# Performance work log

Hardware: AMD Instinct MI355X
Metric: run time of the kernel (lower is better)

The kernel has to match this reference:

```python
import jax, jax.numpy as jnp
import numpy as np

B, C, H, W, HEADS = 8, 256, 64, 64, 4
EPS = 1e-5  # torch InstanceNorm2d default eps


def conv1x1(x, w):
    # w: [out_c, in_c]; x: [b, in_c, h, w]
    return jnp.einsum('oc,bchw->bohw', w, x)


def maxpool2(x):
    b, c, h, w = x.shape
    return x.reshape(b, c, h // 2, 2, w // 2, 2).max(axis=(3, 5))


def inorm_affine(x, g, b):
    # InstanceNorm2d(affine=True): normalize per (batch, channel) over H,W
    m = jnp.mean(x, axis=(2, 3), keepdims=True)
    v = jnp.mean((x - m) ** 2, axis=(2, 3), keepdims=True)
    return (x - m) * jax.lax.rsqrt(v + EPS) * g[None, :, None, None] + b[None, :, None, None]


def setup_inputs() -> dict:
    key = jax.random.key(0)
    ks = jax.random.split(key, 12)
    s = 1.0 / np.sqrt(C)  # fan-in style scaling for 1x1 conv weights
    return {
        'x': jax.random.normal(ks[0], (B, C, H, W), jnp.float32),
        'theta_w': jax.random.normal(ks[1], (C, C), jnp.float32) * s,
        'phi_w': jax.random.normal(ks[2], (C, C), jnp.float32) * s,
        'g_w': jax.random.normal(ks[3], (C // 2, C), jnp.float32) * s,
        'o_w': jax.random.normal(ks[4], (C, C // 2), jnp.float32) * np.sqrt(2.0 / C),
        'nt_w': 1.0 + 0.1 * jax.random.normal(ks[5], (C,), jnp.float32),
        'nt_b': 0.1 * jax.random.normal(ks[6], (C,), jnp.float32),
        'np_w': 1.0 + 0.1 * jax.random.normal(ks[7], (C,), jnp.float32),
        'np_b': 0.1 * jax.random.normal(ks[8], (C,), jnp.float32),
        'ng_w': 1.0 + 0.1 * jax.random.normal(ks[9], (C // 2,), jnp.float32),
        'ng_b': 0.1 * jax.random.normal(ks[10], (C // 2,), jnp.float32),
        'gamma': jnp.float32(0.5),
    }


def reference(x, theta_w, phi_w, g_w, o_w, nt_w, nt_b, np_w, np_b, ng_w, ng_b, gamma):
    b, c, h, w = x.shape
    n = h * w            # query length
    m = n // 4           # key/value length after 2x2 maxpool
    theta = inorm_affine(conv1x1(x, theta_w), nt_w, nt_b)
    phi = inorm_affine(maxpool2(conv1x1(x, phi_w)), np_w, np_b)
    g = inorm_affine(maxpool2(conv1x1(x, g_w)), ng_w, ng_b)
    # custom head layout: channel dim split as (C//heads, heads), head dim INNER
    theta_ = theta.reshape(b, c // HEADS, HEADS, n)
    phi_ = phi.reshape(b, c // HEADS, HEADS, m)
    g_ = g.reshape(b, (c // 2) // HEADS, HEADS, m)
    beta = jax.nn.softmax(jnp.einsum('bchi,bchj->bhij', theta_, phi_), axis=-1)
    o = jnp.einsum('bchj,bhij->bchi', g_, beta).reshape(b, c // 2, h, w)
    o = conv1x1(o, o_w)
    return gamma * o + x
```

## Files before the change

### kernel.cpp

```cpp
#include <hip/hip_runtime.h>
#include <hip/hip_bf16.h>
#include <math.h>

typedef float f32x4 __attribute__((ext_vector_type(4)));
typedef float f32x16 __attribute__((ext_vector_type(16)));
typedef __bf16 b16x8 __attribute__((ext_vector_type(8)));
typedef __bf16 b16x4 __attribute__((ext_vector_type(4)));
typedef unsigned int u32x2 __attribute__((ext_vector_type(2)));
typedef unsigned int u32x4 __attribute__((ext_vector_type(4)));

#define L2E 1.44269504088896340736f

__global__ void prep_weights(const float* tw, const float* pw, const float* gw,
                             const float* ow, __bf16* Wp, __bf16* OWp) {
    int idx = blockIdx.x * 256 + threadIdx.x;
    if (idx < 640 * 256) {
        int m = idx >> 8, k = idx & 255;
        float v;
        if (m < 256)      { int o = ((m & 63) << 2) + (m >> 6);            v = tw[o * 256 + k]; }
        else if (m < 512) { int mm = m - 256; int o = ((mm & 63) << 2) + (mm >> 6); v = pw[o * 256 + k]; }
        else              { int mm = m - 512; int o = ((mm & 31) << 2) + (mm >> 5); v = gw[o * 256 + k]; }
        Wp[idx] = (__bf16)v;
    } else {
        int j = idx - 640 * 256;
        if (j < 256 * 128) {
            int m = j >> 7, c = j & 127;
            int o = ((c & 31) << 2) + (c >> 5);
            OWp[j] = (__bf16)ow[m * 128 + o];
        }
    }
}

__global__ void transpose_x(const float* x, __bf16* xt) {
    __shared__ float tile[32][33];
    int b = blockIdx.z, c0 = blockIdx.y * 32, p0 = blockIdx.x * 32;
    int tx = threadIdx.x & 31, ty = threadIdx.x >> 5;
#pragma unroll
    for (int i = 0; i < 4; i++) {
        int cy = ty + i * 8;
        tile[cy][tx] = x[((size_t)(b * 256 + c0 + cy)) * 4096 + p0 + tx];
    }
    __syncthreads();
#pragma unroll
    for (int i = 0; i < 4; i++) {
        int py = ty + i * 8;
        xt[((size_t)b * 4096 + p0 + py) * 256 + c0 + tx] = (__bf16)tile[tx][py];
    }
}

__global__ __launch_bounds__(256) void conv_gemm(const __bf16* __restrict__ Wp,
                                                 const __bf16* __restrict__ xt,
                                                 __bf16* theta_t, __bf16* phi_t, __bf16* g_t) {
    int b = blockIdx.z, mt = blockIdx.y, nt = blockIdx.x;
    __shared__ __bf16 Al[128 * 40];
    __shared__ __bf16 Bl[128 * 40];
    int tid = threadIdx.x, l = tid & 63, w = tid >> 6;
    int wm = w >> 1, wn = w & 1, lr = l & 15, lg = l >> 4;
    f32x4 acc[4][4];
#pragma unroll
    for (int i = 0; i < 4; i++)
#pragma unroll
        for (int j = 0; j < 4; j++)
#pragma unroll
            for (int r = 0; r < 4; r++) acc[i][j][r] = 0.f;
    const __bf16* Ag = Wp + (size_t)mt * 128 * 256;
    const __bf16* Bg = xt + ((size_t)b * 4096 + nt * 128) * 256;
    int srow = tid >> 2, scol = (tid & 3) * 8;
    b16x8 aR[2], bR[2];
#pragma unroll
    for (int hh = 0; hh < 2; hh++) {
        int r = srow + hh * 64;
        aR[hh] = *(const b16x8*)&Ag[(size_t)r * 256 + scol];
        bR[hh] = *(const b16x8*)&Bg[(size_t)r * 256 + scol];
    }
    for (int k0 = 0; k0 < 256; k0 += 32) {
        if (k0) __syncthreads();
#pragma unroll
        for (int hh = 0; hh < 2; hh++) {
            int r = srow + hh * 64;
            *(b16x8*)&Al[r * 40 + scol] = aR[hh];
            *(b16x8*)&Bl[r * 40 + scol] = bR[hh];
        }
        __syncthreads();
        if (k0 < 224) {
#pragma unroll
            for (int hh = 0; hh < 2; hh++) {
                int r = srow + hh * 64;
                aR[hh] = *(const b16x8*)&Ag[(size_t)r * 256 + k0 + 32 + scol];
                bR[hh] = *(const b16x8*)&Bg[(size_t)r * 256 + k0 + 32 + scol];
            }
        }
        int ko = lg * 8;
        b16x8 af[4], bfr[4];
#pragma unroll
        for (int i = 0; i < 4; i++) af[i]  = *(b16x8*)&Al[(wm * 64 + i * 16 + lr) * 40 + ko];
#pragma unroll
        for (int i = 0; i < 4; i++) bfr[i] = *(b16x8*)&Bl[(wn * 64 + i * 16 + lr) * 40 + ko];
#pragma unroll
        for (int i = 0; i < 4; i++)
#pragma unroll
            for (int j = 0; j < 4; j++)
                acc[i][j] = __builtin_amdgcn_mfma_f32_16x16x32_bf16(af[i], bfr[j], acc[i][j], 0, 0, 0);
    }
    int rbase = lg * 4;
#pragma unroll
    for (int i = 0; i < 4; i++) {
        int m = mt * 128 + wm * 64 + i * 16 + rbase;
#pragma unroll
        for (int j = 0; j < 4; j++) {
            int p = nt * 128 + wn * 64 + j * 16 + lr;
            b16x4 v;
#pragma unroll
            for (int r = 0; r < 4; r++) v[r] = (__bf16)acc[i][j][r];
            if (m < 256)      *(b16x4*)&theta_t[((size_t)b * 4096 + p) * 256 + m] = v;
            else if (m < 512) *(b16x4*)&phi_t[((size_t)b * 4096 + p) * 256 + (m - 256)] = v;
            else              *(b16x4*)&g_t[((size_t)b * 4096 + p) * 128 + (m - 512)] = v;
        }
    }
}

__global__ __launch_bounds__(256) void theta_stats(const __bf16* __restrict__ src,
                                                   float* p1, float* p2) {
    __shared__ float S1[8][256], S2[8][256];
    int b = blockIdx.y, blk = blockIdx.x;
    int tid = threadIdx.x, cg = tid & 31, rg = tid >> 5;
    float a1[8], a2[8];
#pragma unroll
    for (int e = 0; e < 8; e++) { a1[e] = 0.f; a2[e] = 0.f; }
    const __bf16* base = src + ((size_t)b * 4096 + blk * 64 + rg * 8) * 256 + cg * 8;
#pragma unroll
    for (int r = 0; r < 8; r++) {
        b16x8 v = *(const b16x8*)&base[(size_t)r * 256];
#pragma unroll
        for (int e = 0; e < 8; e++) { float f = (float)v[e]; a1[e] += f; a2[e] += f * f; }
    }
#pragma unroll
    for (int e = 0; e < 8; e++) { S1[rg][cg * 8 + e] = a1[e]; S2[rg][cg * 8 + e] = a2[e]; }
    __syncthreads();
    float s1 = 0.f, s2 = 0.f;
#pragma unroll
    for (int i = 0; i < 8; i++) { s1 += S1[i][tid]; s2 += S2[i][tid]; }
    p1[(b * 64 + blk) * 256 + tid] = s1;
    p2[(b * 64 + blk) * 256 + tid] = s2;
}

__global__ __launch_bounds__(256) void pool_phi(const __bf16* __restrict__ src, __bf16* dst,
                                                float* p1, float* p2) {
    __shared__ float S1[8][256], S2[8][256];
    int b = blockIdx.y, qc = blockIdx.x;
    int tid = threadIdx.x, cg = tid & 31, qg = tid >> 5;
    float a1[8], a2[8];
#pragma unroll
    for (int e = 0; e < 8; e++) { a1[e] = 0.f; a2[e] = 0.f; }
#pragma unroll
    for (int qq = 0; qq < 4; qq++) {
        int q = qc * 32 + qg * 4 + qq, qy = q >> 5, qx = q & 31;
        size_t base = ((size_t)(b * 4096) + qy * 128 + qx * 2) * 256 + cg * 8;
        b16x8 v0 = *(const b16x8*)&src[base];
        b16x8 v1 = *(const b16x8*)&src[base + 256];
        b16x8 v2 = *(const b16x8*)&src[base + 16384];
        b16x8 v3 = *(const b16x8*)&src[base + 16640];
        b16x8 mv;
#pragma unroll
        for (int e = 0; e < 8; e++) {
            float m = fmaxf(fmaxf((float)v0[e], (float)v1[e]), fmaxf((float)v2[e], (float)v3[e]));
            mv[e] = (__bf16)m; a1[e] += m; a2[e] += m * m;
        }
        *(b16x8*)&dst[((size_t)b * 1024 + q) * 256 + cg * 8] = mv;
    }
#pragma unroll
    for (int e = 0; e < 8; e++) { S1[qg][cg * 8 + e] = a1[e]; S2[qg][cg * 8 + e] = a2[e]; }
    __syncthreads();
    float s1 = 0.f, s2 = 0.f;
#pragma unroll
    for (int i = 0; i < 8; i++) { s1 += S1[i][tid]; s2 += S2[i][tid]; }
    p1[(b * 32 + qc) * 256 + tid] = s1;
    p2[(b * 32 + qc) * 256 + tid] = s2;
}

__global__ __launch_bounds__(256) void pool_gT(const __bf16* __restrict__ src, __bf16* gT,
                                               float* p1, float* p2) {
    __shared__ __bf16 Pt[64][136];
    __shared__ float S1[16][128], S2[16][128];
    int b = blockIdx.y, qc = blockIdx.x;
    int tid = threadIdx.x, cg = tid & 15, qg = tid >> 4;
    float a1[8], a2[8];
#pragma unroll
    for (int e = 0; e < 8; e++) { a1[e] = 0.f; a2[e] = 0.f; }
#pragma unroll
    for (int qq = 0; qq < 4; qq++) {
        int ql = qg * 4 + qq, q = qc * 64 + ql;
        int qy = q >> 5, qx = q & 31;
        size_t base = ((size_t)(b * 4096) + qy * 128 + qx * 2) * 128 + cg * 8;
        b16x8 v0 = *(const b16x8*)&src[base];
        b16x8 v1 = *(const b16x8*)&src[base + 128];
        b16x8 v2 = *(const b16x8*)&src[base + 8192];
        b16x8 v3 = *(const b16x8*)&src[base + 8320];
        b16x8 mv;
#pragma unroll
        for (int e = 0; e < 8; e++) {
            float m = fmaxf(fmaxf((float)v0[e], (float)v1[e]), fmaxf((float)v2[e], (float)v3[e]));
            mv[e] = (__bf16)m; a1[e] += m; a2[e] += m * m;
        }
        *(b16x8*)&Pt[ql][cg * 8] = mv;
    }
#pragma unroll
    for (int e = 0; e < 8; e++) { S1[qg][cg * 8 + e] = a1[e]; S2[qg][cg * 8 + e] = a2[e]; }
    __syncthreads();
    if (tid < 128) {
        float s1 = 0.f, s2 = 0.f;
#pragma unroll
        for (int i = 0; i < 16; i++) { s1 += S1[i][tid]; s2 += S2[i][tid]; }
        p1[(b * 16 + qc) * 128 + tid] = s1;
        p2[(b * 16 + qc) * 128 + tid] = s2;
    }
    int c = tid & 127, qh = tid >> 7;
    int hh = c >> 5, ch = c & 31;
#pragma unroll
    for (int sg = 0; sg < 4; sg++) {
        int seg = qh * 4 + sg;
        b16x8 v;
#pragma unroll
        for (int e = 0; e < 8; e++) v[e] = Pt[seg * 8 + e][c];
        *(b16x8*)&gT[((((size_t)(b * 4 + hh) * 16 + qc) * 8 + seg) * 32 + ch) * 8] = v;
    }
}

__global__ void finalize_stats(const float* tp1, const float* tp2, const float* pp1,
                               const float* pp2, const float* gp1, const float* gp2,
                               const float* ntw, const float* ntb, const float* npw,
                               const float* npb, const float* ngw, const float* ngb,
                               float* sct, float* bit, float* scp, float* bip,
                               float* scg, float* big) {
    int idx = blockIdx.x * 256 + threadIdx.x;
    if (idx >= 8 * 640) return;
    int b = idx / 640, c = idx % 640;
    if (c < 256) {
        float s1 = 0.f, s2 = 0.f;
        for (int i = 0; i < 64; i++) { s1 += tp1[(b * 64 + i) * 256 + c]; s2 += tp2[(b * 64 + i) * 256 + c]; }
        float n = 4096.f;
        float m = s1 / n, v = s2 / n - m * m;
        float r = rsqrtf(v + 1e-5f);
        int o = ((c & 63) << 2) + (c >> 6);
        float wv = ntw[o], bv = ntb[o];
        sct[b * 256 + c] = r * wv * L2E;
        bit[b * 256 + c] = (bv - m * r * wv) * L2E;
    } else if (c < 512) {
        int cc = c - 256;
        float s1 = 0.f, s2 = 0.f;
        for (int i = 0; i < 32; i++) { s1 += pp1[(b * 32 + i) * 256 + cc]; s2 += pp2[(b * 32 + i) * 256 + cc]; }
        float n = 1024.f;
        float m = s1 / n, v = s2 / n - m * m;
        float r = rsqrtf(v + 1e-5f);
        int o = ((cc & 63) << 2) + (cc >> 6);
        float wv = npw[o], bv = npb[o];
        scp[b * 256 + cc] = r * wv; bip[b * 256 + cc] = bv - m * r * wv;
    } else {
        int cc = c - 512;
        float s1 = 0.f, s2 = 0.f;
        for (int i = 0; i < 16; i++) { s1 += gp1[(b * 16 + i) * 128 + cc]; s2 += gp2[(b * 16 + i) * 128 + cc]; }
        float n = 1024.f;
        float m = s1 / n, v = s2 / n - m * m;
        float r = rsqrtf(v + 1e-5f);
        int o = ((cc & 31) << 2) + (cc >> 5);
        float wv = ngw[o], bv = ngb[o];
        scg[b * 128 + cc] = r * wv; big[b * 128 + cc] = bv - m * r * wv;
    }
}

__global__ void normalize_phi(const __bf16* __restrict__ php, __bf16* __restrict__ phk,
                              const float* __restrict__ scp, const float* __restrict__ bip) {
    int blk = blockIdx.x, t = threadIdx.x;
    int b = blk >> 6, h = (blk >> 4) & 3, cc = blk & 15;
#pragma unroll
    for (int uu = 0; uu < 2; uu++) {
        int u = uu * 256 + t;
        int slot = u >> 6, key = u & 63;
        int q = cc * 64 + key;
        int cfull = h * 64 + (slot >> 1) * 16 + (slot & 1) * 8;
        b16x8 v = *(const b16x8*)&php[((size_t)b * 1024 + q) * 256 + cfull];
        b16x8 nv;
#pragma unroll
        for (int e = 0; e < 8; e++)
            nv[e] = (__bf16)((float)v[e] * scp[b * 256 + cfull + e] + bip[b * 256 + cfull + e]);
        *(b16x8*)&phk[((((size_t)(b * 4 + h) * 16 + cc) * 8 + slot) * 64 + key) * 8] = nv;
    }
}

__global__ __launch_bounds__(256, 2) void attn(const __bf16* __restrict__ theta_t,
                                               const __bf16* __restrict__ phk,
                                               const __bf16* __restrict__ gTz,
                                               const float* __restrict__ sct,
                                               const float* __restrict__ bit,
                                               const float* __restrict__ scg,
                                               const float* __restrict__ big,
                                               __bf16* __restrict__ o_mid) {
    __shared__ __bf16 Kb[2][4096];
    __shared__ __bf16 Vb[2][2048];
    int bid = blockIdx.x;
    int idx = bid >> 3;
    int bh = (bid & 7) * 4 + (idx >> 4), qt = idx & 15;
    int b = bh >> 2, h = bh & 3;
    int tid = threadIdx.x, w = tid >> 6, lane = tid & 63;
    int l31 = lane & 31, hi = lane >> 5;
    int qb = qt * 256 + w * 64;

    b16x8 qf[2][4];
#pragma unroll
    for (int m = 0; m < 2; m++) {
        int q = qb + m * 32 + l31;
        const __bf16* qp = theta_t + ((size_t)b * 4096 + q) * 256 + h * 64;
#pragma unroll
        for (int st = 0; st < 4; st++) {
            int cb = st * 16 + hi * 8;
            b16x8 raw = *(const b16x8*)&qp[cb];
            b16x8 nv;
#pragma unroll
            for (int e = 0; e < 8; e++) {
                int cix = b * 256 + h * 64 + cb + e;
                nv[e] = (__bf16)((float)raw[e] * sct[cix] + bit[cix]);
            }
            qf[m][st] = nv;
        }
    }

    const __bf16* Kg = phk + (size_t)bh * 65536;
    const __bf16* Vg = gTz + (size_t)bh * 32768;

    f32x16 oacc[2];
    float l_run[2] = {0.f, 0.f};
#pragma unroll
    for (int m = 0; m < 2; m++)
#pragma unroll
        for (int r = 0; r < 16; r++) oacc[m][r] = 0.f;
    f32x16 zc;
#pragma unroll
    for (int r = 0; r < 16; r++) zc[r] = 0.f;

#define ISSUE(buf, cc) { \
    __builtin_amdgcn_global_load_lds( \
        (const __attribute__((address_space(1))) void*)(Kg + (size_t)(cc) * 4096 + (w * 2) * 512 + lane * 8), \
        (__attribute__((address_space(3))) void*)(&Kb[buf][(w * 2) * 512]), 16, 0, 0); \
    __builtin_amdgcn_global_load_lds( \
        (const __attribute__((address_space(1))) void*)(Kg + (size_t)(cc) * 4096 + (w * 2 + 1) * 512 + lane * 8), \
        (__attribute__((address_space(3))) void*)(&Kb[buf][(w * 2 + 1) * 512]), 16, 0, 0); \
    __builtin_amdgcn_global_load_lds( \
        (const __attribute__((address_space(1))) void*)(Vg + (size_t)(cc) * 2048 + w * 512 + lane * 8), \
        (__attribute__((address_space(3))) void*)(&Vb[buf][w * 512]), 16, 0, 0); }

#define COMPUTE(cur) { \
    b16x8 ak[2][4], av[4]; \
    _Pragma("unroll") for (int kf = 0; kf < 2; kf++) \
    _Pragma("unroll") for (int st = 0; st < 4; st++) \
        ak[kf][st] = *(b16x8*)&Kb[cur][(st * 2 + hi) * 512 + (kf * 32 + l31) * 8]; \
    _Pragma("unroll") for (int js = 0; js < 4; js++) \
        av[js] = *(b16x8*)&Vb[cur][((js * 2 + hi) * 32 + l31) * 8]; \
    _Pragma("unroll") for (int m = 0; m < 2; m++) { \
        _Pragma("unroll") for (int kf = 0; kf < 2; kf++) { \
            f32x16 s = __builtin_amdgcn_mfma_f32_32x32x16_bf16(ak[kf][0], qf[m][0], zc, 0, 0, 0); \
            _Pragma("unroll") for (int st = 1; st < 4; st++) \
                s = __builtin_amdgcn_mfma_f32_32x32x16_bf16(ak[kf][st], qf[m][st], s, 0, 0, 0); \
            float s0 = 0.f, s1 = 0.f, s2p = 0.f, s3 = 0.f; \
            _Pragma("unroll") for (int r = 0; r < 16; r += 4) { \
                float p0 = __builtin_amdgcn_exp2f(s[r]); \
                float p1 = __builtin_amdgcn_exp2f(s[r + 1]); \
                float p2 = __builtin_amdgcn_exp2f(s[r + 2]); \
                float p3 = __builtin_amdgcn_exp2f(s[r + 3]); \
                s[r] = p0; s[r + 1] = p1; s[r + 2] = p2; s[r + 3] = p3; \
                s0 += p0; s1 += p1; s2p += p2; s3 += p3; \
            } \
            l_run[m] += (s0 + s1) + (s2p + s3); \
            _Pragma("unroll") for (int hh2 = 0; hh2 < 2; hh2++) { \
                b16x4 A4, B4; \
                _Pragma("unroll") for (int e = 0; e < 4; e++) { \
                    A4[e] = (__bf16)s[hh2 * 8 + e]; B4[e] = (__bf16)s[hh2 * 8 + 4 + e]; } \
                u32x2 a2 = __builtin_bit_cast(u32x2, A4); \
                u32x2 b2 = __builtin_bit_cast(u32x2, B4); \
                u32x2 q0 = __builtin_amdgcn_permlane32_swap(a2[0], b2[0], false, false); \
                u32x2 q1 = __builtin_amdgcn_permlane32_swap(a2[1], b2[1], false, false); \
                u32x4 pd = {q0[0], q1[0], q0[1], q1[1]}; \
                b16x8 pf = __builtin_bit_cast(b16x8, pd); \
                oacc[m] = __builtin_amdgcn_mfma_f32_32x32x16_bf16(av[kf * 2 + hh2], pf, oacc[m], 0, 0, 0); \
            } \
        } \
    } }

    ISSUE(0, 0)
    __syncthreads();
#pragma unroll 1
    for (int c = 0; c < 16; c++) {
        if (c < 15) ISSUE((c + 1) & 1, c + 1)
        COMPUTE(c & 1)
        __syncthreads();
    }
#undef ISSUE
#undef COMPUTE

#pragma unroll
    for (int m = 0; m < 2; m++) {
        float lr = l_run[m] + __shfl_xor(l_run[m], 32, 64);
        float rl = 1.0f / lr;
        int q = qb + m * 32 + l31;
#pragma unroll
        for (int rr = 0; rr < 4; rr++) {
            b16x4 v;
#pragma unroll
            for (int e = 0; e < 4; e++) {
                int ci = b * 128 + h * 32 + rr * 8 + hi * 4 + e;
                v[e] = (__bf16)(oacc[m][rr * 4 + e] * rl * scg[ci] + big[ci]);
            }
            *(b16x4*)&o_mid[((size_t)b * 4096 + q) * 128 + h * 32 + rr * 8 + hi * 4] = v;
        }
    }
}

__global__ __launch_bounds__(256) void out_gemm(const __bf16* __restrict__ OWp,
                                                const __bf16* __restrict__ o_mid,
                                                const float* __restrict__ x,
                                                const float* gamma, float* out) {
    int b = blockIdx.z, mt = blockIdx.y, nt = blockIdx.x;
    __shared__ __bf16 Al[128 * 40];
    __shared__ __bf16 Bl[128 * 40];
    int tid = threadIdx.x, l = tid & 63, w = tid >> 6;
    int wm = w >> 1, wn = w & 1, lr = l & 15, lg = l >> 4;
    f32x4 acc[4][4];
#pragma unroll
    for (int i = 0; i < 4; i++)
#pragma unroll
        for (int j = 0; j < 4; j++)
#pragma unroll
            for (int r = 0; r < 4; r++) acc[i][j][r] = 0.f;
    const __bf16* Ag = OWp + (size_t)mt * 128 * 128;
    const __bf16* Bg = o_mid + ((size_t)b * 4096 + nt * 128) * 128;
    int srow = tid >> 2, scol = (tid & 3) * 8;
    b16x8 aR[2], bR[2];
#pragma unroll
    for (int hh = 0; hh < 2; hh++) {
        int r = srow + hh * 64;
        aR[hh] = *(const b16x8*)&Ag[(size_t)r * 128 + scol];
        bR[hh] = *(const b16x8*)&Bg[(size_t)r * 128 + scol];
    }
    for (int k0 = 0; k0 < 128; k0 += 32) {
        if (k0) __syncthreads();
#pragma unroll
        for (int hh = 0; hh < 2; hh++) {
            int r = srow + hh * 64;
            *(b16x8*)&Al[r * 40 + scol] = aR[hh];
            *(b16x8*)&Bl[r * 40 + scol] = bR[hh];
        }
        __syncthreads();
        if (k0 < 96) {
#pragma unroll
            for (int hh = 0; hh < 2; hh++) {
                int r = srow + hh * 64;
                aR[hh] = *(const b16x8*)&Ag[(size_t)r * 128 + k0 + 32 + scol];
                bR[hh] = *(const b16x8*)&Bg[(size_t)r * 128 + k0 + 32 + scol];
            }
        }
        int ko = lg * 8;
        b16x8 af[4], bfr[4];
#pragma unroll
        for (int i = 0; i < 4; i++) af[i]  = *(b16x8*)&Al[(wm * 64 + i * 16 + lr) * 40 + ko];
#pragma unroll
        for (int i = 0; i < 4; i++) bfr[i] = *(b16x8*)&Bl[(wn * 64 + i * 16 + lr) * 40 + ko];
#pragma unroll
        for (int i = 0; i < 4; i++)
#pragma unroll
            for (int j = 0; j < 4; j++)
                acc[i][j] = __builtin_amdgcn_mfma_f32_16x16x32_bf16(af[i], bfr[j], acc[i][j], 0, 0, 0);
    }
    float gm = gamma[0];
    int rbase = lg * 4;
#pragma unroll
    for (int i = 0; i < 4; i++) {
        int m = mt * 128 + wm * 64 + i * 16 + rbase;
#pragma unroll
        for (int j = 0; j < 4; j++) {
            int p = nt * 128 + wn * 64 + j * 16 + lr;
#pragma unroll
            for (int r = 0; r < 4; r++) {
                size_t o = ((size_t)b * 256 + m + r) * 4096 + p;
                out[o] = gm * acc[i][j][r] + x[o];
            }
        }
    }
}

extern "C" void kernel_launch(void* const* d_in, const int* in_sizes, int n_in,
                              void* d_out, int out_size, void* d_ws, size_t ws_size,
                              hipStream_t stream) {
    const float* x   = (const float*)d_in[0];
    const float* tw  = (const float*)d_in[1];
    const float* pw  = (const float*)d_in[2];
    const float* gw  = (const float*)d_in[3];
    const float* ow  = (const float*)d_in[4];
    const float* ntw = (const float*)d_in[5];
    const float* ntb = (const float*)d_in[6];
    const float* npw = (const float*)d_in[7];
    const float* npb = (const float*)d_in[8];
    const float* ngw = (const float*)d_in[9];
    const float* ngb = (const float*)d_in[10];
    const float* gamma = (const float*)d_in[11];
    float* out = (float*)d_out;
    char* ws = (char*)d_ws;

    __bf16* Wp  = (__bf16*)(ws + 0);
    __bf16* OWp = (__bf16*)(ws + 327680);
    __bf16* xt  = (__bf16*)(ws + 393216);
    __bf16* th  = (__bf16*)(ws + 17170432);
    __bf16* phr = (__bf16*)(ws + 33947648);
    __bf16* ghr = (__bf16*)(ws + 50724864);
    __bf16* php = (__bf16*)(ws + 59113472);
    __bf16* gT  = (__bf16*)(ws + 63307776);
    float* sb   = (float*)(ws + 65445888);

    float* tp1 = (float*)(ws + 393216);
    float* tp2 = (float*)(ws + 917504);
    float* pp1 = (float*)(ws + 1441792);
    float* pp2 = (float*)(ws + 1703936);
    float* gp1 = (float*)(ws + 1966080);
    float* gp2 = (float*)(ws + 2031616);
    __bf16* phk = phr;
    __bf16* om  = xt;

    float *sct = sb, *bit = sb + 2048, *scp = sb + 4096, *bip = sb + 6144,
          *scg = sb + 8192, *big = sb + 9216;

    prep_weights<<<768, 256, 0, stream>>>(tw, pw, gw, ow, Wp, OWp);
    transpose_x<<<dim3(128, 8, 8), 256, 0, stream>>>(x, xt);
    conv_gemm<<<dim3(32, 5, 8), 256, 0, stream>>>(Wp, xt, th, phr, ghr);
    theta_stats<<<dim3(64, 8), 256, 0, stream>>>(th, tp1, tp2);
    pool_phi<<<dim3(32, 8), 256, 0, stream>>>(phr, php, pp1, pp2);
    pool_gT<<<dim3(16, 8), 256, 0, stream>>>(ghr, gT, gp1, gp2);
    finalize_stats<<<20, 256, 0, stream>>>(tp1, tp2, pp1, pp2, gp1, gp2,
                                           ntw, ntb, npw, npb, ngw, ngb,
                                           sct, bit, scp, bip, scg, big);
    normalize_phi<<<512, 256, 0, stream>>>(php, phk, scp, bip);
    attn<<<512, 256, 0, stream>>>(th, phk, gT, sct, bit, scg, big, om);
    out_gemm<<<dim3(32, 2, 8), 256, 0, stream>>>(OWp, om, x, gamma, out);
}
```

Measured before the change: 124.5 us.

## Fuse x transpose into conv GEMM and triple-buffer attention with smaller query tiles

Removes the separate transpose_x kernel: conv_gemm now reads fp32 x directly in channel-major order, converts it to bf16 and writes the transposed tile into LDS. The attention kernel halves the query tile per wave (one 32-row fragment instead of two), doubling the grid to 1024 blocks. It also switches K/V staging to a three-buffer ring with explicit vmcnt waits and a single barrier per step. This cuts a full-tensor round trip and aims to improve latency hiding and occupancy. The cost is more K/V reloads per query and less reuse of each loaded tile.

After: 120.2 us. 1.04x faster.

```diff
diff --git a/kernel.cpp b/kernel.cpp
--- a/kernel.cpp
+++ b/kernel.cpp
@@ -31,25 +31,8 @@
     }
 }
 
-__global__ void transpose_x(const float* x, __bf16* xt) {
-    __shared__ float tile[32][33];
-    int b = blockIdx.z, c0 = blockIdx.y * 32, p0 = blockIdx.x * 32;
-    int tx = threadIdx.x & 31, ty = threadIdx.x >> 5;
-#pragma unroll
-    for (int i = 0; i < 4; i++) {
-        int cy = ty + i * 8;
-        tile[cy][tx] = x[((size_t)(b * 256 + c0 + cy)) * 4096 + p0 + tx];
-    }
-    __syncthreads();
-#pragma unroll
-    for (int i = 0; i < 4; i++) {
-        int py = ty + i * 8;
-        xt[((size_t)b * 4096 + p0 + py) * 256 + c0 + tx] = (__bf16)tile[tx][py];
-    }
-}
-
 __global__ __launch_bounds__(256) void conv_gemm(const __bf16* __restrict__ Wp,
-                                                 const __bf16* __restrict__ xt,
+                                                 const float* __restrict__ x,
                                                  __bf16* theta_t, __bf16* phi_t, __bf16* g_t) {
     int b = blockIdx.z, mt = blockIdx.y, nt = blockIdx.x;
     __shared__ __bf16 Al[128 * 40];
@@ -64,31 +47,41 @@
 #pragma unroll
             for (int r = 0; r < 4; r++) acc[i][j][r] = 0.f;
     const __bf16* Ag = Wp + (size_t)mt * 128 * 256;
-    const __bf16* Bg = xt + ((size_t)b * 4096 + nt * 128) * 256;
+    const float* Bx = x + (size_t)b * 1048576 + nt * 128;
     int srow = tid >> 2, scol = (tid & 3) * 8;
-    b16x8 aR[2], bR[2];
-#pragma unroll
-    for (int hh = 0; hh < 2; hh++) {
-        int r = srow + hh * 64;
-        aR[hh] = *(const b16x8*)&Ag[(size_t)r * 256 + scol];
-        bR[hh] = *(const b16x8*)&Bg[(size_t)r * 256 + scol];
-    }
+    int bn = tid & 127, bk0 = (tid >> 7) * 8;
+    b16x8 aR[2];
+    float xr[2][8];
+#pragma unroll
+    for (int hh = 0; hh < 2; hh++)
+        aR[hh] = *(const b16x8*)&Ag[(size_t)(srow + hh * 64) * 256 + scol];
+#pragma unroll
+    for (int u = 0; u < 2; u++)
+#pragma unroll
+        for (int e = 0; e < 8; e++)
+            xr[u][e] = Bx[(size_t)(bk0 + u * 16 + e) * 4096 + bn];
     for (int k0 = 0; k0 < 256; k0 += 32) {
         if (k0) __syncthreads();
 #pragma unroll
-        for (int hh = 0; hh < 2; hh++) {
-            int r = srow + hh * 64;
-            *(b16x8*)&Al[r * 40 + scol] = aR[hh];
-            *(b16x8*)&Bl[r * 40 + scol] = bR[hh];
+        for (int hh = 0; hh < 2; hh++)
+            *(b16x8*)&Al[(srow + hh * 64) * 40 + scol] = aR[hh];
+#pragma unroll
+        for (int u = 0; u < 2; u++) {
+            b16x8 v;
+#pragma unroll
+            for (int e = 0; e < 8; e++) v[e] = (__bf16)xr[u][e];
+            *(b16x8*)&Bl[bn * 40 + bk0 + u * 16] = v;
         }
         __syncthreads();
         if (k0 < 224) {
 #pragma unroll
-            for (int hh = 0; hh < 2; hh++) {
-                int r = srow + hh * 64;
-                aR[hh] = *(const b16x8*)&Ag[(size_t)r * 256 + k0 + 32 + scol];
-                bR[hh] = *(const b16x8*)&Bg[(size_t)r * 256 + k0 + 32 + scol];
-            }
+            for (int hh = 0; hh < 2; hh++)
+                aR[hh] = *(const b16x8*)&Ag[(size_t)(srow + hh * 64) * 256 + k0 + 32 + scol];
+#pragma unroll
+            for (int u = 0; u < 2; u++)
+#pragma unroll
+                for (int e = 0; e < 8; e++)
+                    xr[u][e] = Bx[(size_t)(k0 + 32 + bk0 + u * 16 + e) * 4096 + bn];
         }
         int ko = lg * 8;
         b16x8 af[4], bfr[4];
@@ -295,20 +288,18 @@
                                                const float* __restrict__ scg,
                                                const float* __restrict__ big,
                                                __bf16* __restrict__ o_mid) {
-    __shared__ __bf16 Kb[2][4096];
-    __shared__ __bf16 Vb[2][2048];
+    __shared__ __bf16 Kb[3][4096];
+    __shared__ __bf16 Vb[3][2048];
     int bid = blockIdx.x;
     int idx = bid >> 3;
-    int bh = (bid & 7) * 4 + (idx >> 4), qt = idx & 15;
+    int bh = (bid & 7) * 4 + (idx >> 5), qt = idx & 31;
     int b = bh >> 2, h = bh & 3;
     int tid = threadIdx.x, w = tid >> 6, lane = tid & 63;
     int l31 = lane & 31, hi = lane >> 5;
-    int qb = qt * 256 + w * 64;
-
-    b16x8 qf[2][4];
-#pragma unroll
-    for (int m = 0; m < 2; m++) {
-        int q = qb + m * 32 + l31;
+    int q = qt * 128 + w * 32 + l31;
+
+    b16x8 qf[4];
+    {
         const __bf16* qp = theta_t + ((size_t)b * 4096 + q) * 256 + h * 64;
 #pragma unroll
         for (int st = 0; st < 4; st++) {
@@ -320,19 +311,17 @@
                 int cix = b * 256 + h * 64 + cb + e;
                 nv[e] = (__bf16)((float)raw[e] * sct[cix] + bit[cix]);
             }
-            qf[m][st] = nv;
+            qf[st] = nv;
         }
     }
 
     const __bf16* Kg = phk + (size_t)bh * 65536;
     const __bf16* Vg = gTz + (size_t)bh * 32768;
 
-    f32x16 oacc[2];
-    float l_run[2] = {0.f, 0.f};
-#pragma unroll
-    for (int m = 0; m < 2; m++)
-#pragma unroll
-        for (int r = 0; r < 16; r++) oacc[m][r] = 0.f;
+    f32x16 oacc;
+    float l_run = 0.f;
+#pragma unroll
+    for (int r = 0; r < 16; r++) oacc[r] = 0.f;
     f32x16 zc;
 #pragma unroll
     for (int r = 0; r < 16; r++) zc[r] = 0.f;
@@ -355,59 +344,58 @@
         ak[kf][st] = *(b16x8*)&Kb[cur][(st * 2 + hi) * 512 + (kf * 32 + l31) * 8]; \
     _Pragma("unroll") for (int js = 0; js < 4; js++) \
         av[js] = *(b16x8*)&Vb[cur][((js * 2 + hi) * 32 + l31) * 8]; \
-    _Pragma("unroll") for (int m = 0; m < 2; m++) { \
-        _Pragma("unroll") for (int kf = 0; kf < 2; kf++) { \
-            f32x16 s = __builtin_amdgcn_mfma_f32_32x32x16_bf16(ak[kf][0], qf[m][0], zc, 0, 0, 0); \
-            _Pragma("unroll") for (int st = 1; st < 4; st++) \
-                s = __builtin_amdgcn_mfma_f32_32x32x16_bf16(ak[kf][st], qf[m][st], s, 0, 0, 0); \
-            float s0 = 0.f, s1 = 0.f, s2p = 0.f, s3 = 0.f; \
-            _Pragma("unroll") for (int r = 0; r < 16; r += 4) { \
-                float p0 = __builtin_amdgcn_exp2f(s[r]); \
-                float p1 = __builtin_amdgcn_exp2f(s[r + 1]); \
-                float p2 = __builtin_amdgcn_exp2f(s[r + 2]); \
-                float p3 = __builtin_amdgcn_exp2f(s[r + 3]); \
-                s[r] = p0; s[r + 1] = p1; s[r + 2] = p2; s[r + 3] = p3; \
-                s0 += p0; s1 += p1; s2p += p2; s3 += p3; \
-            } \
-            l_run[m] += (s0 + s1) + (s2p + s3); \
-            _Pragma("unroll") for (int hh2 = 0; hh2 < 2; hh2++) { \
-                b16x4 A4, B4; \
-                _Pragma("unroll") for (int e = 0; e < 4; e++) { \
-                    A4[e] = (__bf16)s[hh2 * 8 + e]; B4[e] = (__bf16)s[hh2 * 8 + 4 + e]; } \
-                u32x2 a2 = __builtin_bit_cast(u32x2, A4); \
-                u32x2 b2 = __builtin_bit_cast(u32x2, B4); \
-                u32x2 q0 = __builtin_amdgcn_permlane32_swap(a2[0], b2[0], false, false); \
-                u32x2 q1 = __builtin_amdgcn_permlane32_swap(a2[1], b2[1], false, false); \
-                u32x4 pd = {q0[0], q1[0], q0[1], q1[1]}; \
-                b16x8 pf = __builtin_bit_cast(b16x8, pd); \
-                oacc[m] = __builtin_amdgcn_mfma_f32_32x32x16_bf16(av[kf * 2 + hh2], pf, oacc[m], 0, 0, 0); \
-            } \
+    _Pragma("unroll") for (int kf = 0; kf < 2; kf++) { \
+        f32x16 s = __builtin_amdgcn_mfma_f32_32x32x16_bf16(ak[kf][0], qf[0], zc, 0, 0, 0); \
+        _Pragma("unroll") for (int st = 1; st < 4; st++) \
+            s = __builtin_amdgcn_mfma_f32_32x32x16_bf16(ak[kf][st], qf[st], s, 0, 0, 0); \
+        float s0 = 0.f, s1 = 0.f, s2p = 0.f, s3 = 0.f; \
+        _Pragma("unroll") for (int r = 0; r < 16; r += 4) { \
+            float p0 = __builtin_amdgcn_exp2f(s[r]); \
+            float p1 = __builtin_amdgcn_exp2f(s[r + 1]); \
+            float p2 = __builtin_amdgcn_exp2f(s[r + 2]); \
+            float p3 = __builtin_amdgcn_exp2f(s[r + 3]); \
+            s[r] = p0; s[r + 1] = p1; s[r + 2] = p2; s[r + 3] = p3; \
+            s0 += p0; s1 += p1; s2p += p2; s3 += p3; \
+        } \
+        l_run += (s0 + s1) + (s2p + s3); \
+        _Pragma("unroll") for (int hh2 = 0; hh2 < 2; hh2++) { \
+            b16x4 A4, B4; \
+            _Pragma("unroll") for (int e = 0; e < 4; e++) { \
+                A4[e] = (__bf16)s[hh2 * 8 + e]; B4[e] = (__bf16)s[hh2 * 8 + 4 + e]; } \
+            u32x2 a2 = __builtin_bit_cast(u32x2, A4); \
+            u32x2 b2 = __builtin_bit_cast(u32x2, B4); \
+            u32x2 q0 = __builtin_amdgcn_permlane32_swap(a2[0], b2[0], false, false); \
+            u32x2 q1 = __builtin_amdgcn_permlane32_swap(a2[1], b2[1], false, false); \
+            u32x4 pd = {q0[0], q1[0], q0[1], q1[1]}; \
+            b16x8 pf = __builtin_bit_cast(b16x8, pd); \
+            oacc = __builtin_amdgcn_mfma_f32_32x32x16_bf16(av[kf * 2 + hh2], pf, oacc, 0, 0, 0); \
         } \
     } }
 
     ISSUE(0, 0)
-    __syncthreads();
+    ISSUE(1, 1)
 #pragma unroll 1
     for (int c = 0; c < 16; c++) {
-        if (c < 15) ISSUE((c + 1) & 1, c + 1)
-        COMPUTE(c & 1)
-        __syncthreads();
+        if (c < 15) { asm volatile("s_waitcnt vmcnt(3)" ::: "memory"); }
+        else        { asm volatile("s_waitcnt vmcnt(0)" ::: "memory"); }
+        __builtin_amdgcn_s_barrier();
+        __builtin_amdgcn_sched_barrier(0);
+        if (c + 2 < 16) { int ib = (c + 2) % 3; ISSUE(ib, c + 2) }
+        COMPUTE(c % 3)
     }
 #undef ISSUE
 #undef COMPUTE
 
-#pragma unroll
-    for (int m = 0; m < 2; m++) {
-        float lr = l_run[m] + __shfl_xor(l_run[m], 32, 64);
+    {
+        float lr = l_run + __shfl_xor(l_run, 32, 64);
         float rl = 1.0f / lr;
-        int q = qb + m * 32 + l31;
 #pragma unroll
         for (int rr = 0; rr < 4; rr++) {
             b16x4 v;
 #pragma unroll
             for (int e = 0; e < 4; e++) {
                 int ci = b * 128 + h * 32 + rr * 8 + hi * 4 + e;
-                v[e] = (__bf16)(oacc[m][rr * 4 + e] * rl * scg[ci] + big[ci]);
+                v[e] = (__bf16)(oacc[rr * 4 + e] * rl * scg[ci] + big[ci]);
             }
             *(b16x4*)&o_mid[((size_t)b * 4096 + q) * 128 + h * 32 + rr * 8 + hi * 4] = v;
         }
@@ -506,7 +494,6 @@
 
     __bf16* Wp  = (__bf16*)(ws + 0);
     __bf16* OWp = (__bf16*)(ws + 327680);
-    __bf16* xt  = (__bf16*)(ws + 393216);
     __bf16* th  = (__bf16*)(ws + 17170432);
     __bf16* phr = (__bf16*)(ws + 33947648);
     __bf16* ghr = (__bf16*)(ws + 50724864);
@@ -521,14 +508,13 @@
     float* gp1 = (float*)(ws + 1966080);
     float* gp2 = (float*)(ws + 2031616);
     __bf16* phk = phr;
-    __bf16* om  = xt;
+    __bf16* om  = (__bf16*)(ws + 2097152);
 
     float *sct = sb, *bit = sb + 2048, *scp = sb + 4096, *bip = sb + 6144,
           *scg = sb + 8192, *big = sb + 9216;
 
     prep_weights<<<768, 256, 0, stream>>>(tw, pw, gw, ow, Wp, OWp);
-    transpose_x<<<dim3(128, 8, 8), 256, 0, stream>>>(x, xt);
-    conv_gemm<<<dim3(32, 5, 8), 256, 0, stream>>>(Wp, xt, th, phr, ghr);
+    conv_gemm<<<dim3(32, 5, 8), 256, 0, stream>>>(Wp, x, th, phr, ghr);
     theta_stats<<<dim3(64, 8), 256, 0, stream>>>(th, tp1, tp2);
     pool_phi<<<dim3(32, 8), 256, 0, stream>>>(phr, php, pp1, pp2);
     pool_gT<<<dim3(16, 8), 256, 0, stream>>>(ghr, gT, gp1, gp2);
@@ -536,6 +522,6 @@
                                            ntw, ntb, npw, npb, ngw, ngb,
                                            sct, bit, scp, bip, scg, big);
     normalize_phi<<<512, 256, 0, stream>>>(php, phk, scp, bip);
-    attn<<<512, 256, 0, stream>>>(th, phk, gT, sct, bit, scg, big, om);
+    attn<<<1024, 256, 0, stream>>>(th, phk, gT, sct, bit, scg, big, om);
     out_gemm<<<dim3(32, 2, 8), 256, 0, stream>>>(OWp, om, x, gamma, out);
 }
```
